# Optimization experiments

Measured on AMD Instinct MI355X. Metric: run time of the kernel, lower is better.

## Reference

```python
import jax, jax.numpy as jnp
import numpy as np

B, T, IN, H = 64, 512, 128, 512


def _lstm_layer(x, W_ih, W_hh, b_ih, b_hh):
    """Single unidirectional LSTM layer, batch_first input x: [B,T,in].
    PyTorch gate order: i, f, g, o. Returns outputs [B,T,H]."""
    # Precompute input contribution for all timesteps: [T,B,4H]
    xg = jnp.einsum('bti,gi->tbg', x, W_ih) + (b_ih + b_hh)
    Bt = x.shape[0]
    h0 = jnp.zeros((Bt, W_hh.shape[1]), x.dtype)
    c0 = jnp.zeros_like(h0)

    def step(carry, xt):
        h, c = carry
        g = xt + h @ W_hh.T  # [B,4H]
        i, f, gg, o = jnp.split(g, 4, axis=-1)
        i = jax.nn.sigmoid(i)
        f = jax.nn.sigmoid(f)
        gg = jnp.tanh(gg)
        o = jax.nn.sigmoid(o)
        c = f * c + i * gg
        h = o * jnp.tanh(c)
        return (h, c), h

    (_, _), hs = jax.lax.scan(step, (h0, c0), xg)
    return jnp.transpose(hs, (1, 0, 2))  # [B,T,H]


def setup_inputs() -> dict:
    key = jax.random.key(0)
    ks = jax.random.split(key, 11)
    s_in = 1.0 / np.sqrt(H)  # PyTorch LSTM init scale U(-1/sqrt(H), 1/sqrt(H))
    u = lambda k, shape: jax.random.uniform(k, shape, jnp.float32, -s_in, s_in)
    return {
        'x': jax.random.normal(ks[0], (B, T, IN), jnp.float32),
        'W_ih0': u(ks[1], (4 * H, IN)),
        'W_hh0': u(ks[2], (4 * H, H)),
        'b_ih0': u(ks[3], (4 * H,)),
        'b_hh0': u(ks[4], (4 * H,)),
        'W_ih1': u(ks[5], (4 * H, H)),
        'W_hh1': u(ks[6], (4 * H, H)),
        'b_ih1': u(ks[7], (4 * H,)),
        'b_hh1': u(ks[8], (4 * H,)),
        'W_fc': u(ks[9], (1, H)),
        'b_fc': u(ks[10], (1,)),
    }


def reference(x, W_ih0, W_hh0, b_ih0, b_hh0, W_ih1, W_hh1, b_ih1, b_hh1, W_fc, b_fc):
    out = _lstm_layer(x, W_ih0, W_hh0, b_ih0, b_hh0)
    out = _lstm_layer(out, W_ih1, W_hh1, b_ih1, b_hh1)
    logits = out[:, -1, :] @ W_fc.T + b_fc  # [B,1]
    return logits
```

## Files before the change

kernel.cpp:

```cpp
#include <hip/hip_runtime.h>


#define NWG 64
#define NB 64
#define NT 512
#define NH 512
#define BLK 512
#define SREC (NWG * BLK)

typedef float f32x4 __attribute__((ext_vector_type(4)));
typedef __bf16 bf16x4 __attribute__((ext_vector_type(4)));
typedef __bf16 bf16x8 __attribute__((ext_vector_type(8)));
typedef unsigned long long u64;
typedef unsigned u32;

__device__ __forceinline__ bf16x4 ld8_bypass(const __bf16* p) {
    u64 v = __hip_atomic_load((const u64*)p, __ATOMIC_RELAXED, __HIP_MEMORY_SCOPE_AGENT);
    bf16x4 r; __builtin_memcpy(&r, &v, 8); return r;
}
__device__ __forceinline__ void st8_bypass(__bf16* p, u64 v) {
    __hip_atomic_store((u64*)p, v, __ATOMIC_RELAXED, __HIP_MEMORY_SCOPE_AGENT);
}

__device__ __forceinline__ void wait_flags(const unsigned* flags, unsigned target, int lane) {
    int g = 0;
    for (;;) {
        unsigned f = __hip_atomic_load((unsigned*)&flags[lane],
                                       __ATOMIC_RELAXED, __HIP_MEMORY_SCOPE_AGENT);
        if (__all((int)(f >= target))) break;
        if (++g > (1 << 17)) break;
    }
}

__device__ __forceinline__ unsigned short bfbits(float f) {
    __bf16 h = (__bf16)f; unsigned short u; __builtin_memcpy(&u, &h, 2); return u;
}

__global__ void prep_kernel(unsigned short* hinit, unsigned short* hs1, unsigned* fl) {
    int i = blockIdx.x * blockDim.x + threadIdx.x;
    if (i < SREC) hinit[i] = 0;
    if (i < 2 * SREC) hs1[i] = 0;
    if (i < 128) fl[i] = 0;
}

template<int KIH, int IS_L0>
__device__ __forceinline__ void layer_body(
    char* Wl, float (*gbuf)[36], unsigned short (*hstage)[8],
    int wg,
    const float* __restrict__ W_ih, const float* __restrict__ W_hh,
    const float* __restrict__ b_ih, const float* __restrict__ b_hh,
    const float* __restrict__ x_f32,
    __bf16* __restrict__ h0_all,
    const __bf16* __restrict__ hinit,
    __bf16* __restrict__ hbuf,
    float* __restrict__ h_final,
    unsigned* __restrict__ flags_self,
    const unsigned* __restrict__ flags_dep)
{
    constexpr int KTOT = KIH + NH;
    constexpr int NCH_A = KIH / 32;
    constexpr int NCH_B = NH / 32;
    constexpr int ROWB = KTOT * 2;

    const int tid = threadIdx.x;
    const int hcol0 = wg * 8;

    {
        constexpr int CPR = KTOT / 8;
        for (int cid = tid; cid < 32 * CPR; cid += 512) {
            const int r = cid / CPR;
            const int k0 = (cid - r * CPR) * 8;
            const int grow = (r >> 3) * NH + hcol0 + (r & 7);
            const float* src = (k0 < KIH) ? (W_ih + (size_t)grow * KIH + k0)
                                          : (W_hh + (size_t)grow * NH + (k0 - KIH));
            union { __bf16 h[8]; uint4 u; } tmp;
            #pragma unroll
            for (int j = 0; j < 8; ++j) tmp.h[j] = (__bf16)src[j];
            const unsigned off = (unsigned)(r * ROWB) +
                (((unsigned)(2 * k0)) ^ ((unsigned)((r & 7) << 4)));
            *(uint4*)(Wl + off) = tmp.u;
        }
    }

    const int eb = tid >> 3, ec = tid & 7;
    const int hcE = hcol0 + ec;
    const float bI = b_ih[hcE]          + b_hh[hcE];
    const float bF = b_ih[NH + hcE]     + b_hh[NH + hcE];
    const float bG = b_ih[2 * NH + hcE] + b_hh[2 * NH + hcE];
    const float bO = b_ih[3 * NH + hcE] + b_hh[3 * NH + hcE];
    float creg = 0.0f;
    __syncthreads();

    const int lane = tid & 63;
    const int wid = tid >> 6;
    const int bt = (wid & 3) * 16;
    const int gt = (wid >> 2) * 16;
    const int arow = bt + (lane & 15);
    const int q4 = ((lane >> 4) & 3) * 4;
    const int brow = gt + (lane & 15);
    const char* wrow = Wl + brow * ROWB;
    const unsigned bsz = (unsigned)((brow & 7) << 4);

    const int aoff = arow * 8 + (q4 & 4);
    const int bsub = (q4 >> 3);

    auto wfrag = [&](int k0) -> bf16x8 {
        const bf16x4 blo = *(const bf16x4*)(wrow + (((unsigned)(2 * (k0 + q4))) ^ bsz));
        const bf16x4 bhi = *(const bf16x4*)(wrow + (((unsigned)(2 * (k0 + 16 + q4))) ^ bsz));
        return __builtin_shufflevector(blo, bhi, 0, 1, 2, 3, 4, 5, 6, 7);
    };

    for (int t = 0; t < NT; ++t) {
        const __bf16* __restrict__ hprev;
        __bf16* __restrict__ hout;
        if constexpr (IS_L0 != 0) {
            hprev = (t == 0) ? hinit : (h0_all + (size_t)(t - 1) * SREC);
            hout = h0_all + (size_t)t * SREC;
        } else {
            hprev = hbuf + (size_t)(t & 1) * SREC;
            hout = hbuf + (size_t)((t + 1) & 1) * SREC;
        }

        f32x4 accA0 = {0.f,0.f,0.f,0.f}, accA1 = {0.f,0.f,0.f,0.f};
        f32x4 accB0 = {0.f,0.f,0.f,0.f}, accB1 = {0.f,0.f,0.f,0.f};

        if constexpr (IS_L0 != 0) {
            const float* xb = x_f32 + ((size_t)arow * NT + t) * KIH;
            bf16x8 av[NCH_A];
            #pragma unroll
            for (int kk = 0; kk < NCH_A; ++kk) {
                const float4 lo = *(const float4*)(xb + kk * 32 + q4);
                const float4 hi = *(const float4*)(xb + kk * 32 + 16 + q4);
                const bf16x4 alo = {(__bf16)lo.x, (__bf16)lo.y, (__bf16)lo.z, (__bf16)lo.w};
                const bf16x4 ahi = {(__bf16)hi.x, (__bf16)hi.y, (__bf16)hi.z, (__bf16)hi.w};
                av[kk] = __builtin_shufflevector(alo, ahi, 0, 1, 2, 3, 4, 5, 6, 7);
            }
            #pragma unroll
            for (int kk = 0; kk < NCH_A; ++kk) {
                f32x4& a = (kk & 1) ? accA1 : accA0;
                a = __builtin_amdgcn_mfma_f32_16x16x32_bf16(av[kk], wfrag(kk * 32), a, 0, 0, 0);
            }
            if (t > 0 && wid == 0) wait_flags(flags_self, (unsigned)t, lane);
            __syncthreads();
        } else {
            if (wid == 0) wait_flags(flags_dep, (unsigned)(t + 1), lane);
            if (wid == 1 && t > 0) wait_flags(flags_self, (unsigned)t, lane);
            __syncthreads();
        }

        bf16x4 aBlo[NCH_B], aBhi[NCH_B];
        #pragma unroll
        for (int kk = 0; kk < NCH_B; ++kk) {
            const __bf16* base = hprev + (4 * kk + bsub) * BLK + aoff;
            aBlo[kk] = ld8_bypass(base);
            aBhi[kk] = ld8_bypass(base + 2 * BLK);
        }
        if constexpr (IS_L0 == 0) {
            const __bf16* hA = h0_all + (size_t)t * SREC;
            bf16x4 aAlo[NCH_A], aAhi[NCH_A];
            #pragma unroll
            for (int kk = 0; kk < NCH_A; ++kk) {
                const __bf16* base = hA + (4 * kk + bsub) * BLK + aoff;
                aAlo[kk] = ld8_bypass(base);
                aAhi[kk] = ld8_bypass(base + 2 * BLK);
            }
            #pragma unroll
            for (int kk = 0; kk < NCH_A; ++kk) {
                f32x4& a = (kk & 1) ? accA1 : accA0;
                const bf16x8 av = __builtin_shufflevector(aAlo[kk], aAhi[kk], 0,1,2,3,4,5,6,7);
                a = __builtin_amdgcn_mfma_f32_16x16x32_bf16(av, wfrag(kk * 32), a, 0, 0, 0);
            }
        }
        #pragma unroll
        for (int kk = 0; kk < NCH_B; ++kk) {
            f32x4& a = (kk & 1) ? accB1 : accB0;
            const bf16x8 av = __builtin_shufflevector(aBlo[kk], aBhi[kk], 0,1,2,3,4,5,6,7);
            a = __builtin_amdgcn_mfma_f32_16x16x32_bf16(av, wfrag(KIH + kk * 32), a, 0, 0, 0);
        }

        const f32x4 acc = (accA0 + accA1) + (accB0 + accB1);

        #pragma unroll
        for (int i = 0; i < 4; ++i)
            gbuf[bt + ((lane >> 4) & 3) * 4 + i][gt + (lane & 15)] = acc[i];
        __syncthreads();

        {
            const float gi = gbuf[eb][ec]      + bI;
            const float gf = gbuf[eb][8 + ec]  + bF;
            const float gg = gbuf[eb][16 + ec] + bG;
            const float go = gbuf[eb][24 + ec] + bO;
            const float ii = 1.0f / (1.0f + __expf(-gi));
            const float ff = 1.0f / (1.0f + __expf(-gf));
            const float g2 = 2.0f / (1.0f + __expf(-2.0f * gg)) - 1.0f;
            const float oo = 1.0f / (1.0f + __expf(-go));
            const float cn = ff * creg + ii * g2;
            const float th = 2.0f / (1.0f + __expf(-2.0f * cn)) - 1.0f;
            const float hn = oo * th;
            creg = cn;
            hstage[eb][ec] = bfbits(hn);
            if constexpr (IS_L0 == 0) {
                if (t == NT - 1) h_final[(size_t)eb * NH + hcol0 + ec] = hn;
            }
        }
        __syncthreads();

        if (tid < 128) {
            u64 v;
            __builtin_memcpy(&v, &hstage[tid >> 1][(tid & 1) * 4], 8);
            st8_bypass(hout + (size_t)wg * BLK + tid * 4, v);
        }
        asm volatile("s_waitcnt vmcnt(0)" ::: "memory");
        __syncthreads();
        if (tid == 0)
            __hip_atomic_store(&flags_self[wg], (unsigned)(t + 1),
                               __ATOMIC_RELAXED, __HIP_MEMORY_SCOPE_AGENT);
    }
}

__launch_bounds__(512, 2)
__global__ void lstm_fused_kernel(
    const float* W_ih0, const float* W_hh0, const float* b_ih0, const float* b_hh0,
    const float* W_ih1, const float* W_hh1, const float* b_ih1, const float* b_hh1,
    const float* x, __bf16* h0_all, __bf16* hinit, __bf16* hs1,
    float* hfin, unsigned* fl0, unsigned* fl1)
{
    __shared__ __align__(16) char Wl[32 * 2048];
    __shared__ float gbuf[64][36];
    __shared__ unsigned short hstage[64][8];

    if (blockIdx.x < NWG) {
        layer_body<128, 1>(Wl, gbuf, hstage, blockIdx.x,
                           W_ih0, W_hh0, b_ih0, b_hh0,
                           x, h0_all, hinit, nullptr, nullptr, fl0, nullptr);
    } else {
        layer_body<512, 0>(Wl, gbuf, hstage, blockIdx.x - NWG,
                           W_ih1, W_hh1, b_ih1, b_hh1,
                           nullptr, h0_all, hinit, hs1, hfin, fl1, fl0);
    }
}

__global__ void fc_kernel(const float* __restrict__ hfin,
                          const float* __restrict__ w_fc,
                          const float* __restrict__ b_fc,
                          float* __restrict__ out) {
    __shared__ float red[64][9];
    const int tid = threadIdx.x;
    const int b = tid >> 3, p = tid & 7;
    const int k0 = p * 64;
    float s = 0.f;
    #pragma unroll 8
    for (int k = 0; k < 64; ++k) s += hfin[(size_t)b * NH + k0 + k] * w_fc[k0 + k];
    red[b][p] = s;
    __syncthreads();
    if (p == 0) {
        float a = 0.f;
        #pragma unroll
        for (int j = 0; j < 8; ++j) a += red[b][j];
        out[b] = a + b_fc[0];
    }
}

extern "C" void kernel_launch(void* const* d_in, const int* in_sizes, int n_in,
                              void* d_out, int out_size, void* d_ws, size_t ws_size,
                              hipStream_t stream) {
    const float* x     = (const float*)d_in[0];
    const float* W_ih0 = (const float*)d_in[1];
    const float* W_hh0 = (const float*)d_in[2];
    const float* b_ih0 = (const float*)d_in[3];
    const float* b_hh0 = (const float*)d_in[4];
    const float* W_ih1 = (const float*)d_in[5];
    const float* W_hh1 = (const float*)d_in[6];
    const float* b_ih1 = (const float*)d_in[7];
    const float* b_hh1 = (const float*)d_in[8];
    const float* W_fc  = (const float*)d_in[9];
    const float* b_fc  = (const float*)d_in[10];

    char* ws = (char*)d_ws;
    __bf16*  h0_all = (__bf16*)(ws);
    __bf16*  hinit  = (__bf16*)(ws + 33554432);
    __bf16*  hs1    = (__bf16*)(ws + 33554432 + 65536);
    float*   hfin   = (float*) (ws + 33554432 + 196608);
    unsigned* fl0   = (unsigned*)(ws + 33554432 + 327680);
    unsigned* fl1   = fl0 + 64;

    prep_kernel<<<dim3(256), dim3(256), 0, stream>>>(
        (unsigned short*)hinit, (unsigned short*)hs1, fl0);

    lstm_fused_kernel<<<dim3(2 * NWG), dim3(512), 0, stream>>>(
        W_ih0, W_hh0, b_ih0, b_hh0, W_ih1, W_hh1, b_ih1, b_hh1,
        x, h0_all, hinit, hs1, hfin, fl0, fl1);

    fc_kernel<<<dim3(1), dim3(512), 0, stream>>>(hfin, W_fc, b_fc, (float*)d_out);
}
```

Baseline: 3.888 ms.

## Halve workgroup size, reuse each h fragment across two gate tiles, pad flags

Each workgroup drops from 8 waves to 4. Each wave now covers all 32 gate columns for its 16 batch rows by issuing two MFMAs per A fragment. This halves the duplicated global loads of the previous h and x per step, and each elementwise thread now handles two hidden columns with a packed 32-bit staging write. Per-workgroup sync flags are padded 16 words apart to avoid false sharing during polling. The cost is a longer serial MFMA chain per wave and fewer waves to hide latency in this latency-bound recurrence.

```diff
diff --git a/kernel.cpp b/kernel.cpp
--- a/kernel.cpp
+++ b/kernel.cpp
@@ -7,6 +7,7 @@
 #define NH 512
 #define BLK 512
 #define SREC (NWG * BLK)
+#define FPAD 16
 
 typedef float f32x4 __attribute__((ext_vector_type(4)));
 typedef __bf16 bf16x4 __attribute__((ext_vector_type(4)));
@@ -25,7 +26,7 @@
 __device__ __forceinline__ void wait_flags(const unsigned* flags, unsigned target, int lane) {
     int g = 0;
     for (;;) {
-        unsigned f = __hip_atomic_load((unsigned*)&flags[lane],
+        unsigned f = __hip_atomic_load((unsigned*)&flags[lane * FPAD],
                                        __ATOMIC_RELAXED, __HIP_MEMORY_SCOPE_AGENT);
         if (__all((int)(f >= target))) break;
         if (++g > (1 << 17)) break;
@@ -40,12 +41,12 @@
     int i = blockIdx.x * blockDim.x + threadIdx.x;
     if (i < SREC) hinit[i] = 0;
     if (i < 2 * SREC) hs1[i] = 0;
-    if (i < 128) fl[i] = 0;
+    if (i < 2 * NWG * FPAD) fl[i] = 0;
 }
 
 template<int KIH, int IS_L0>
 __device__ __forceinline__ void layer_body(
-    char* Wl, float (*gbuf)[36], unsigned short (*hstage)[8],
+    char* Wl, float (*gbuf)[36], u32 (*hstage32)[4],
     int wg,
     const float* __restrict__ W_ih, const float* __restrict__ W_hh,
     const float* __restrict__ b_ih, const float* __restrict__ b_hh,
@@ -67,7 +68,7 @@
 
     {
         constexpr int CPR = KTOT / 8;
-        for (int cid = tid; cid < 32 * CPR; cid += 512) {
+        for (int cid = tid; cid < 32 * CPR; cid += 256) {
             const int r = cid / CPR;
             const int k0 = (cid - r * CPR) * 8;
             const int grow = (r >> 3) * NH + hcol0 + (r & 7);
@@ -82,32 +83,37 @@
         }
     }
 
-    const int eb = tid >> 3, ec = tid & 7;
-    const int hcE = hcol0 + ec;
-    const float bI = b_ih[hcE]          + b_hh[hcE];
-    const float bF = b_ih[NH + hcE]     + b_hh[NH + hcE];
-    const float bG = b_ih[2 * NH + hcE] + b_hh[2 * NH + hcE];
-    const float bO = b_ih[3 * NH + hcE] + b_hh[3 * NH + hcE];
-    float creg = 0.0f;
+    const int eb = tid >> 2, ecp = (tid & 3) * 2;
+    float bI[2], bF[2], bG[2], bO[2];
+    #pragma unroll
+    for (int j = 0; j < 2; ++j) {
+        const int c = hcol0 + ecp + j;
+        bI[j] = b_ih[c] + b_hh[c];
+        bF[j] = b_ih[NH + c] + b_hh[NH + c];
+        bG[j] = b_ih[2 * NH + c] + b_hh[2 * NH + c];
+        bO[j] = b_ih[3 * NH + c] + b_hh[3 * NH + c];
+    }
+    float c0 = 0.f, c1 = 0.f;
     __syncthreads();
 
     const int lane = tid & 63;
     const int wid = tid >> 6;
-    const int bt = (wid & 3) * 16;
-    const int gt = (wid >> 2) * 16;
+    const int bt = wid * 16;
     const int arow = bt + (lane & 15);
     const int q4 = ((lane >> 4) & 3) * 4;
-    const int brow = gt + (lane & 15);
-    const char* wrow = Wl + brow * ROWB;
-    const unsigned bsz = (unsigned)((brow & 7) << 4);
-
+    const char* wrow0 = Wl + (lane & 15) * ROWB;
+    const char* wrow1 = wrow0 + 16 * ROWB;
+    const unsigned bsz = (unsigned)((lane & 7) << 4);
     const int aoff = arow * 8 + (q4 & 4);
     const int bsub = (q4 >> 3);
 
-    auto wfrag = [&](int k0) -> bf16x8 {
-        const bf16x4 blo = *(const bf16x4*)(wrow + (((unsigned)(2 * (k0 + q4))) ^ bsz));
-        const bf16x4 bhi = *(const bf16x4*)(wrow + (((unsigned)(2 * (k0 + 16 + q4))) ^ bsz));
-        return __builtin_shufflevector(blo, bhi, 0, 1, 2, 3, 4, 5, 6, 7);
+    auto wfragp = [&](const char* wr, int k0) -> bf16x8 {
+        const bf16x4 lo = *(const bf16x4*)(wr + (((unsigned)(2 * (k0 + q4))) ^ bsz));
+        const bf16x4 hi = *(const bf16x4*)(wr + (((unsigned)(2 * (k0 + 16 + q4))) ^ bsz));
+        return __builtin_shufflevector(lo, hi, 0, 1, 2, 3, 4, 5, 6, 7);
+    };
+    auto mk8 = [&](bf16x4 lo, bf16x4 hi) -> bf16x8 {
+        return __builtin_shufflevector(lo, hi, 0, 1, 2, 3, 4, 5, 6, 7);
     };
 
     for (int t = 0; t < NT; ++t) {
@@ -121,24 +127,22 @@
             hout = hbuf + (size_t)((t + 1) & 1) * SREC;
         }
 
-        f32x4 accA0 = {0.f,0.f,0.f,0.f}, accA1 = {0.f,0.f,0.f,0.f};
-        f32x4 accB0 = {0.f,0.f,0.f,0.f}, accB1 = {0.f,0.f,0.f,0.f};
+        f32x4 p0a = {0,0,0,0}, p0b = {0,0,0,0};
+        f32x4 p1a = {0,0,0,0}, p1b = {0,0,0,0};
 
         if constexpr (IS_L0 != 0) {
             const float* xb = x_f32 + ((size_t)arow * NT + t) * KIH;
-            bf16x8 av[NCH_A];
             #pragma unroll
             for (int kk = 0; kk < NCH_A; ++kk) {
                 const float4 lo = *(const float4*)(xb + kk * 32 + q4);
                 const float4 hi = *(const float4*)(xb + kk * 32 + 16 + q4);
                 const bf16x4 alo = {(__bf16)lo.x, (__bf16)lo.y, (__bf16)lo.z, (__bf16)lo.w};
                 const bf16x4 ahi = {(__bf16)hi.x, (__bf16)hi.y, (__bf16)hi.z, (__bf16)hi.w};
-                av[kk] = __builtin_shufflevector(alo, ahi, 0, 1, 2, 3, 4, 5, 6, 7);
-            }
-            #pragma unroll
-            for (int kk = 0; kk < NCH_A; ++kk) {
-                f32x4& a = (kk & 1) ? accA1 : accA0;
-                a = __builtin_amdgcn_mfma_f32_16x16x32_bf16(av[kk], wfrag(kk * 32), a, 0, 0, 0);
+                const bf16x8 av = mk8(alo, ahi);
+                f32x4& d0 = (kk & 1) ? p0b : p0a;
+                d0 = __builtin_amdgcn_mfma_f32_16x16x32_bf16(av, wfragp(wrow0, kk * 32), d0, 0, 0, 0);
+                f32x4& d1 = (kk & 1) ? p1b : p1a;
+                d1 = __builtin_amdgcn_mfma_f32_16x16x32_bf16(av, wfragp(wrow1, kk * 32), d1, 0, 0, 0);
             }
             if (t > 0 && wid == 0) wait_flags(flags_self, (unsigned)t, lane);
             __syncthreads();
@@ -166,59 +170,72 @@
             }
             #pragma unroll
             for (int kk = 0; kk < NCH_A; ++kk) {
-                f32x4& a = (kk & 1) ? accA1 : accA0;
-                const bf16x8 av = __builtin_shufflevector(aAlo[kk], aAhi[kk], 0,1,2,3,4,5,6,7);
-                a = __builtin_amdgcn_mfma_f32_16x16x32_bf16(av, wfrag(kk * 32), a, 0, 0, 0);
+                const bf16x8 av = mk8(aAlo[kk], aAhi[kk]);
+                f32x4& d0 = (kk & 1) ? p0b : p0a;
+                d0 = __builtin_amdgcn_mfma_f32_16x16x32_bf16(av, wfragp(wrow0, kk * 32), d0, 0, 0, 0);
+                f32x4& d1 = (kk & 1) ? p1b : p1a;
+                d1 = __builtin_amdgcn_mfma_f32_16x16x32_bf16(av, wfragp(wrow1, kk * 32), d1, 0, 0, 0);
             }
         }
         #pragma unroll
         for (int kk = 0; kk < NCH_B; ++kk) {
-            f32x4& a = (kk & 1) ? accB1 : accB0;
-            const bf16x8 av = __builtin_shufflevector(aBlo[kk], aBhi[kk], 0,1,2,3,4,5,6,7);
-            a = __builtin_amdgcn_mfma_f32_16x16x32_bf16(av, wfrag(KIH + kk * 32), a, 0, 0, 0);
-        }
-
-        const f32x4 acc = (accA0 + accA1) + (accB0 + accB1);
-
+            const bf16x8 av = mk8(aBlo[kk], aBhi[kk]);
+            f32x4& d0 = (kk & 1) ? p0b : p0a;
+            d0 = __builtin_amdgcn_mfma_f32_16x16x32_bf16(av, wfragp(wrow0, KIH + kk * 32), d0, 0, 0, 0);
+            f32x4& d1 = (kk & 1) ? p1b : p1a;
+            d1 = __builtin_amdgcn_mfma_f32_16x16x32_bf16(av, wfragp(wrow1, KIH + kk * 32), d1, 0, 0, 0);
+        }
+
+        const f32x4 s0 = p0a + p0b, s1 = p1a + p1b;
         #pragma unroll
-        for (int i = 0; i < 4; ++i)
-            gbuf[bt + ((lane >> 4) & 3) * 4 + i][gt + (lane & 15)] = acc[i];
+        for (int i = 0; i < 4; ++i) {
+            gbuf[bt + ((lane >> 4) & 3) * 4 + i][lane & 15]        = s0[i];
+            gbuf[bt + ((lane >> 4) & 3) * 4 + i][16 + (lane & 15)] = s1[i];
+        }
         __syncthreads();
 
         {
-            const float gi = gbuf[eb][ec]      + bI;
-            const float gf = gbuf[eb][8 + ec]  + bF;
-            const float gg = gbuf[eb][16 + ec] + bG;
-            const float go = gbuf[eb][24 + ec] + bO;
-            const float ii = 1.0f / (1.0f + __expf(-gi));
-            const float ff = 1.0f / (1.0f + __expf(-gf));
-            const float g2 = 2.0f / (1.0f + __expf(-2.0f * gg)) - 1.0f;
-            const float oo = 1.0f / (1.0f + __expf(-go));
-            const float cn = ff * creg + ii * g2;
-            const float th = 2.0f / (1.0f + __expf(-2.0f * cn)) - 1.0f;
-            const float hn = oo * th;
-            creg = cn;
-            hstage[eb][ec] = bfbits(hn);
+            float hh[2]; float cc[2] = {c0, c1};
+            #pragma unroll
+            for (int j = 0; j < 2; ++j) {
+                const int c = ecp + j;
+                const float gi = gbuf[eb][c]      + bI[j];
+                const float gf = gbuf[eb][8 + c]  + bF[j];
+                const float gg = gbuf[eb][16 + c] + bG[j];
+                const float go = gbuf[eb][24 + c] + bO[j];
+                const float ii = 1.f / (1.f + __expf(-gi));
+                const float ff = 1.f / (1.f + __expf(-gf));
+                const float g2 = 2.f / (1.f + __expf(-2.f * gg)) - 1.f;
+                const float oo = 1.f / (1.f + __expf(-go));
+                const float cn = ff * cc[j] + ii * g2;
+                const float th = 2.f / (1.f + __expf(-2.f * cn)) - 1.f;
+                hh[j] = oo * th;
+                cc[j] = cn;
+            }
+            c0 = cc[0]; c1 = cc[1];
+            hstage32[eb][tid & 3] = (u32)bfbits(hh[0]) | ((u32)bfbits(hh[1]) << 16);
             if constexpr (IS_L0 == 0) {
-                if (t == NT - 1) h_final[(size_t)eb * NH + hcol0 + ec] = hn;
+                if (t == NT - 1) {
+                    h_final[(size_t)eb * NH + hcol0 + ecp]     = hh[0];
+                    h_final[(size_t)eb * NH + hcol0 + ecp + 1] = hh[1];
+                }
             }
         }
         __syncthreads();
 
         if (tid < 128) {
-            u64 v;
-            __builtin_memcpy(&v, &hstage[tid >> 1][(tid & 1) * 4], 8);
+            const u64 v = ((const u64*)hstage32)[tid];
             st8_bypass(hout + (size_t)wg * BLK + tid * 4, v);
         }
         asm volatile("s_waitcnt vmcnt(0)" ::: "memory");
         __syncthreads();
         if (tid == 0)
-            __hip_atomic_store(&flags_self[wg], (unsigned)(t + 1),
+            __hip_atomic_store(&flags_self[wg * FPAD], (unsigned)(t + 1),
                                __ATOMIC_RELAXED, __HIP_MEMORY_SCOPE_AGENT);
     }
 }
 
-__launch_bounds__(512, 2)
+__launch_bounds__(256, 2)
 __global__ void lstm_fused_kernel(
     const float* W_ih0, const float* W_hh0, const float* b_ih0, const float* b_hh0,
     const float* W_ih1, const float* W_hh1, const float* b_ih1, const float* b_hh1,
@@ -227,14 +244,14 @@
 {
     __shared__ __align__(16) char Wl[32 * 2048];
     __shared__ float gbuf[64][36];
-    __shared__ unsigned short hstage[64][8];
+    __shared__ u32 hstage32[64][4];
 
     if (blockIdx.x < NWG) {
-        layer_body<128, 1>(Wl, gbuf, hstage, blockIdx.x,
+        layer_body<128, 1>(Wl, gbuf, hstage32, blockIdx.x,
                            W_ih0, W_hh0, b_ih0, b_hh0,
                            x, h0_all, hinit, nullptr, nullptr, fl0, nullptr);
     } else {
-        layer_body<512, 0>(Wl, gbuf, hstage, blockIdx.x - NWG,
+        layer_body<512, 0>(Wl, gbuf, hstage32, blockIdx.x - NWG,
                            W_ih1, W_hh1, b_ih1, b_hh1,
                            nullptr, h0_all, hinit, hs1, hfin, fl1, fl0);
     }
@@ -282,12 +299,12 @@
     __bf16*  hs1    = (__bf16*)(ws + 33554432 + 65536);
     float*   hfin   = (float*) (ws + 33554432 + 196608);
     unsigned* fl0   = (unsigned*)(ws + 33554432 + 327680);
-    unsigned* fl1   = fl0 + 64;
+    unsigned* fl1   = fl0 + NWG * FPAD;
 
     prep_kernel<<<dim3(256), dim3(256), 0, stream>>>(
         (unsigned short*)hinit, (unsigned short*)hs1, fl0);
 
-    lstm_fused_kernel<<<dim3(2 * NWG), dim3(512), 0, stream>>>(
+    lstm_fused_kernel<<<dim3(2 * NWG), dim3(256), 0, stream>>>(
         W_ih0, W_hh0, b_ih0, b_hh0, W_ih1, W_hh1, b_ih1, b_hh1,
         x, h0_all, hinit, hs1, hfin, fl0, fl1);
 
```

New measurement: 3.123 ms. -19.7%, faster.
